# Optimization experiments

Hardware: AMD Instinct MI355X
Metric: run time of the kernel (lower is better)

The kernel has to match this reference:

```python
import jax, jax.numpy as jnp
import numpy as np

NUM_HEADS = 16
SOFTPLUS_EPS = 1e-4


def rotate_half(x):
    x1, x2 = jnp.split(x, 2, axis=-1)
    return jnp.concatenate((-x2, x1), axis=-1)


def setup_inputs() -> dict:
    key = jax.random.key(0)
    B, S, H = 1, 2048, 2048
    D = H // NUM_HEADS  # 128
    ks = jax.random.split(key, 5)
    hidden_states = jax.random.normal(ks[0], (B, S, H), dtype=jnp.float32)
    # standard RoPE tables: [S, D]
    inv_freq = 1.0 / (10000.0 ** (np.arange(0, D, 2, dtype=np.float32) / D))
    freqs = np.outer(np.arange(S, dtype=np.float32), inv_freq)  # [S, D/2]
    emb = np.concatenate([freqs, freqs], axis=-1)  # [S, D]
    cos = jnp.asarray(np.cos(emb), dtype=jnp.float32)
    sin = jnp.asarray(np.sin(emb), dtype=jnp.float32)
    std = 0.02
    w_q = jax.random.normal(ks[1], (2 * H, H), dtype=jnp.float32) * std
    w_k = jax.random.normal(ks[2], (2 * H, H), dtype=jnp.float32) * std
    w_v = jax.random.normal(ks[3], (H, H), dtype=jnp.float32) * std
    w_o = jax.random.normal(ks[4], (H, H), dtype=jnp.float32) * std
    return {"hidden_states": hidden_states, "cos": cos, "sin": sin,
            "w_q": w_q, "w_k": w_k, "w_v": w_v, "w_o": w_o}


def reference(hidden_states, cos, sin, w_q, w_k, w_v, w_o):
    B, S, H = hidden_states.shape
    NH = NUM_HEADS
    D = H // NH
    # projections (torch Linear: y = x @ W.T)
    q = (hidden_states @ w_q.T).reshape(B, S, NH, 2 * D).swapaxes(1, 2)  # [B,NH,S,2D]
    k = (hidden_states @ w_k.T).reshape(B, S, NH, 2 * D).swapaxes(1, 2)
    v = (hidden_states @ w_v.T).reshape(B, S, NH, D).swapaxes(1, 2)      # [B,NH,S,D]
    q_mu, q_sigma_raw = jnp.split(q, 2, axis=-1)
    k_mu, k_sigma_raw = jnp.split(k, 2, axis=-1)
    q_sigma = jax.nn.softplus(q_sigma_raw) + SOFTPLUS_EPS
    k_sigma = jax.nn.softplus(k_sigma_raw) + SOFTPLUS_EPS
    q_w = q_mu / jnp.sqrt(q_sigma)
    k_w = k_mu / jnp.sqrt(k_sigma)
    # RoPE on variance-weighted means; cos/sin [S,D] broadcast over [B,NH,S,D]
    q_w = q_w * cos + rotate_half(q_w) * sin
    k_w = k_w * cos + rotate_half(k_w) * sin
    q_sq = jnp.sum(q_w * q_w, axis=-1, keepdims=True)          # [B,NH,S,1]
    k_sq = jnp.sum(k_w * k_w, axis=-1, keepdims=True)          # [B,NH,S,1]
    dot = jnp.einsum('bhqd,bhkd->bhqk', q_w, k_w)              # [B,NH,S,S]
    weighted_dist = q_sq + jnp.swapaxes(k_sq, -2, -1) - 2.0 * dot
    log_det_q = jnp.sum(jnp.log(q_sigma), axis=-1, keepdims=True)
    log_det_k = jnp.sum(jnp.log(k_sigma), axis=-1, keepdims=True)
    log_det = log_det_q + jnp.swapaxes(log_det_k, -2, -1)
    attn_scores = -0.5 * (weighted_dist + log_det)
    attn_probs = jax.nn.softmax(attn_scores, axis=-1)
    attn_out = jnp.einsum('bhqk,bhkd->bhqd', attn_probs, v)    # [B,NH,S,D]
    attn_out = attn_out.swapaxes(1, 2).reshape(B, S, H)
    return attn_out @ w_o.T
```

## Files before the change

kernel.cpp:

```cpp
#include <hip/hip_runtime.h>
#include <stdint.h>

#define S_LEN 2048
#define HID   2048
#define NHEAD 16
#define HD    128
#define NQK   8192
#define K_HID 2048

typedef _Float16 f16x8 __attribute__((ext_vector_type(8)));
typedef float    f32x4 __attribute__((ext_vector_type(4)));

__device__ __forceinline__ unsigned short f2h(float f) {
    _Float16 h = (_Float16)f;
    union { _Float16 h; unsigned short u; } c; c.h = h;
    return c.u;
}
__device__ __forceinline__ float h2f(unsigned short b) {
    union { unsigned short u; _Float16 h; } c; c.u = b;
    return (float)c.h;
}
__device__ __forceinline__ float softplus_f(float x) {
    return (x > 20.f) ? x : log1pf(expf(x));
}
__device__ __forceinline__ void gload_lds16(const unsigned short* g, unsigned short* l) {
    __builtin_amdgcn_global_load_lds(
        (const __attribute__((address_space(1))) unsigned int*)g,
        (__attribute__((address_space(3))) unsigned int*)l, 16, 0, 0);
}
__device__ __forceinline__ void bar() {
    asm volatile("" ::: "memory");
    __builtin_amdgcn_s_barrier();
    asm volatile("" ::: "memory");
}
#define VMCNT(n) asm volatile("s_waitcnt vmcnt(" #n ")" ::: "memory")

__global__ __launch_bounds__(256) void cast5(const float* __restrict__ hs,
                                             const float* __restrict__ wq,
                                             const float* __restrict__ wk,
                                             const float* __restrict__ wv,
                                             const float* __restrict__ wo,
                                             unsigned short* __restrict__ hs16,
                                             unsigned short* __restrict__ wqk16,
                                             unsigned short* __restrict__ wv16,
                                             unsigned short* __restrict__ wo16) {
    int b = blockIdx.x;
    const float* src;
    unsigned short* dst;
    int i;
    if (b < 4096)       { src = hs; dst = hs16;                          i = b; }
    else if (b < 12288) { src = wq; dst = wqk16;                         i = b - 4096; }
    else if (b < 20480) { src = wk; dst = wqk16 + (size_t)4096 * K_HID;  i = b - 12288; }
    else if (b < 24576) { src = wv; dst = wv16;                          i = b - 20480; }
    else                { src = wo; dst = wo16;                          i = b - 24576; }
    int idx = i * 256 + threadIdx.x;
    float4 v = ((const float4*)src)[idx];
    ushort4 o;
    o.x = f2h(v.x); o.y = f2h(v.y); o.z = f2h(v.z); o.w = f2h(v.w);
    ((ushort4*)dst)[idx] = o;
}

template <bool OUT_F16>
__device__ __forceinline__ void gemm_body(const unsigned short* __restrict__ A,
                                          const unsigned short* __restrict__ B,
                                          void* __restrict__ Cv,
                                          int m0, int n0, int N,
                                          unsigned short* As, unsigned short* Bs) {
    const int t    = threadIdx.x;
    const int wave = t >> 6;
    const int lane = t & 63;
    const int wm   = wave >> 1, wn = wave & 1;
    const int lrow = lane & 15, quad = lane >> 4;
    const int srow = lane >> 2;
    const int scol = (lane & 3) * 8;

    f32x4 acc[4][4];
    for (int i = 0; i < 4; ++i)
        for (int j = 0; j < 4; ++j)
            acc[i][j] = (f32x4){0.f, 0.f, 0.f, 0.f};

    for (int k0 = 0; k0 < K_HID; k0 += 32) {
        for (int c = 0; c < 2; ++c) {
            int ch = wave * 2 + c;
            int row = ch * 16 + srow;
            gload_lds16(A + (size_t)(m0 + row) * K_HID + k0 + scol, &As[ch * 512]);
            gload_lds16(B + (size_t)(n0 + row) * K_HID + k0 + scol, &Bs[ch * 512]);
        }
        __syncthreads();

        f16x8 af[4], bfr[4];
        for (int tm = 0; tm < 4; ++tm)
            af[tm]  = *(const f16x8*)(&As[(wm * 64 + tm * 16 + lrow) * 32 + quad * 8]);
        for (int tn = 0; tn < 4; ++tn)
            bfr[tn] = *(const f16x8*)(&Bs[(wn * 64 + tn * 16 + lrow) * 32 + quad * 8]);
        for (int tm = 0; tm < 4; ++tm)
            for (int tn = 0; tn < 4; ++tn)
                acc[tm][tn] = __builtin_amdgcn_mfma_f32_16x16x32_f16(af[tm], bfr[tn], acc[tm][tn], 0, 0, 0);
        __syncthreads();
    }

    for (int tm = 0; tm < 4; ++tm)
        for (int tn = 0; tn < 4; ++tn) {
            int col = n0 + wn * 64 + tn * 16 + lrow;
            for (int r = 0; r < 4; ++r) {
                int row = m0 + wm * 64 + tm * 16 + quad * 4 + r;
                if (OUT_F16)
                    ((unsigned short*)Cv)[(size_t)row * N + col] = f2h(acc[tm][tn][r]);
                else
                    ((float*)Cv)[(size_t)row * N + col] = acc[tm][tn][r];
            }
        }
}

__global__ __launch_bounds__(256) void gemm_qkv(const unsigned short* __restrict__ hs16,
                                                const unsigned short* __restrict__ wqk16,
                                                const unsigned short* __restrict__ wv16,
                                                unsigned short* __restrict__ qk16,
                                                unsigned short* __restrict__ Vt) {
    __shared__ __align__(16) unsigned short As[128 * 32];
    __shared__ __align__(16) unsigned short Bs[128 * 32];
    int b = blockIdx.x;
    if (b < 1024) {
        gemm_body<true>(hs16, wqk16, qk16, (b >> 6) * 128, (b & 63) * 128, NQK, As, Bs);
    } else {
        b -= 1024;
        gemm_body<true>(wv16, hs16, Vt, (b >> 4) * 128, (b & 15) * 128, S_LEN, As, Bs);
    }
}

template <bool OUT_F16>
__global__ __launch_bounds__(256) void gemm_nt_f16(const unsigned short* __restrict__ A,
                                                   const unsigned short* __restrict__ B,
                                                   void* __restrict__ Cv,
                                                   int M, int N, int Kd) {
    __shared__ __align__(16) unsigned short As[128 * 32];
    __shared__ __align__(16) unsigned short Bs[128 * 32];
    gemm_body<OUT_F16>(A, B, Cv, blockIdx.y * 128, blockIdx.x * 128, N, As, Bs);
}

__global__ __launch_bounds__(512, 2) void gemm256_qk(const unsigned short* __restrict__ A,
                                                     const unsigned short* __restrict__ B,
                                                     unsigned short* __restrict__ C) {
    extern __shared__ __align__(16) unsigned short lds[];
    const int t    = threadIdx.x;
    const int wave = t >> 6;
    const int lane = t & 63;
    const int wm   = wave >> 2, wn = wave & 3;
    const int lrow = lane & 15, quad = lane >> 4;

    const int x  = blockIdx.x & 7;
    const int sl = blockIdx.x >> 3;
    const int tm = ((x >> 2) << 2) + (sl >> 3);
    const int tn = ((x & 3) << 3) + (sl & 7);
    const int m0 = tm << 8, n0 = tn << 8;

    const int srow = lane >> 2;
    const int scol = ((lane & 3) * 8) ^ ((lane >> 5) << 4);
    const unsigned short* Ag = A + (size_t)(m0 + wave * 16 + srow) * K_HID + scol;
    const unsigned short* Bg = B + (size_t)(n0 + wave * 16 + srow) * K_HID + scol;

    const int swz = (lrow * 32 + quad * 8) ^ ((lrow >> 3) << 4);

    f32x4 acc[8][4];
    #pragma unroll
    for (int i = 0; i < 8; ++i)
        #pragma unroll
        for (int j = 0; j < 4; ++j) acc[i][j] = (f32x4){0.f, 0.f, 0.f, 0.f};

    {
        unsigned short* la = lds + wave * 1024;
        gload_lds16(Ag,               la);
        gload_lds16(Ag + 32,          la + 512);
        gload_lds16(Ag + 262144,      la + 8192);
        gload_lds16(Ag + 262144 + 32, la + 8704);
        unsigned short* lb = la + 16384;
        gload_lds16(Bg,               lb);
        gload_lds16(Bg + 32,          lb + 512);
        gload_lds16(Bg + 262144,      lb + 8192);
        gload_lds16(Bg + 262144 + 32, lb + 8704);
    }
    VMCNT(0);
    bar();

    f16x8 ah[4][2], b01[2][2];

    const int NT = K_HID / 64;
    #pragma unroll 1
    for (int t2 = 0; t2 < NT; ++t2) {
        const int buf = t2 & 1;
        const unsigned short* Lb = lds + buf * 32768;
        unsigned short*       Ln = lds + (buf ^ 1) * 32768 + wave * 1024;
        const int k1  = (t2 + 1) * 64;
        const bool pre = (t2 < NT - 1);

        f16x8 al[4][2], b23[2][2];

        if (pre) {
            gload_lds16(Ag + k1,               Ln);
            gload_lds16(Ag + k1 + 32,          Ln + 512);
            gload_lds16(Ag + 262144 + k1,      Ln + 8192);
            gload_lds16(Ag + 262144 + k1 + 32, Ln + 8704);
        }
        #pragma unroll
        for (int i = 0; i < 4; ++i) {
            al[i][0] = *(const f16x8*)(Lb + (wm * 8 + i) * 1024 + swz);
            al[i][1] = *(const f16x8*)(Lb + (wm * 8 + i) * 1024 + 512 + swz);
        }
        if (t2) {
            __builtin_amdgcn_s_setprio(1);
            #pragma unroll
            for (int i = 0; i < 4; ++i)
                #pragma unroll
                for (int j = 0; j < 2; ++j) {
                    acc[4 + i][j] = __builtin_amdgcn_mfma_f32_16x16x32_f16(ah[i][0], b01[j][0], acc[4 + i][j], 0, 0, 0);
                    acc[4 + i][j] = __builtin_amdgcn_mfma_f32_16x16x32_f16(ah[i][1], b01[j][1], acc[4 + i][j], 0, 0, 0);
                }
            __builtin_amdgcn_s_setprio(0);
        }
        #pragma unroll
        for (int j = 0; j < 2; ++j) {
            b01[j][0] = *(const f16x8*)(Lb + 16384 + (wn * 4 + j) * 1024 + swz);
            b01[j][1] = *(const f16x8*)(Lb + 16384 + (wn * 4 + j) * 1024 + 512 + swz);
        }
        bar();

        if (pre) {
            gload_lds16(Bg + k1,               Ln + 16384);
            gload_lds16(Bg + k1 + 32,          Ln + 16896);
            gload_lds16(Bg + 262144 + k1,      Ln + 24576);
            gload_lds16(Bg + 262144 + k1 + 32, Ln + 25088);
        }
        #pragma unroll
        for (int j = 0; j < 2; ++j) {
            b23[j][0] = *(const f16x8*)(Lb + 16384 + (wn * 4 + 2 + j) * 1024 + swz);
            b23[j][1] = *(const f16x8*)(Lb + 16384 + (wn * 4 + 2 + j) * 1024 + 512 + swz);
        }
        __builtin_amdgcn_s_setprio(1);
        #pragma unroll
        for (int i = 0; i < 4; ++i)
            #pragma unroll
            for (int j = 0; j < 2; ++j) {
                acc[i][j] = __builtin_amdgcn_mfma_f32_16x16x32_f16(al[i][0], b01[j][0], acc[i][j], 0, 0, 0);
                acc[i][j] = __builtin_amdgcn_mfma_f32_16x16x32_f16(al[i][1], b01[j][1], acc[i][j], 0, 0, 0);
            }
        __builtin_amdgcn_s_setprio(0);
        bar();

        #pragma unroll
        for (int i = 0; i < 4; ++i) {
            ah[i][0] = *(const f16x8*)(Lb + (wm * 8 + 4 + i) * 1024 + swz);
            ah[i][1] = *(const f16x8*)(Lb + (wm * 8 + 4 + i) * 1024 + 512 + swz);
        }
        __builtin_amdgcn_s_setprio(1);
        #pragma unroll
        for (int i = 0; i < 4; ++i)
            #pragma unroll
            for (int j = 0; j < 2; ++j) {
                acc[i][2 + j] = __builtin_amdgcn_mfma_f32_16x16x32_f16(al[i][0], b23[j][0], acc[i][2 + j], 0, 0, 0);
                acc[i][2 + j] = __builtin_amdgcn_mfma_f32_16x16x32_f16(al[i][1], b23[j][1], acc[i][2 + j], 0, 0, 0);
            }
        __builtin_amdgcn_s_setprio(0);
        bar();

        __builtin_amdgcn_s_setprio(1);
        #pragma unroll
        for (int i = 0; i < 4; ++i)
            #pragma unroll
            for (int j = 0; j < 2; ++j) {
                acc[4 + i][2 + j] = __builtin_amdgcn_mfma_f32_16x16x32_f16(ah[i][0], b23[j][0], acc[4 + i][2 + j], 0, 0, 0);
                acc[4 + i][2 + j] = __builtin_amdgcn_mfma_f32_16x16x32_f16(ah[i][1], b23[j][1], acc[4 + i][2 + j], 0, 0, 0);
            }
        __builtin_amdgcn_s_setprio(0);
        VMCNT(0);
        bar();
    }

    __builtin_amdgcn_s_setprio(1);
    #pragma unroll
    for (int i = 0; i < 4; ++i)
        #pragma unroll
        for (int j = 0; j < 2; ++j) {
            acc[4 + i][j] = __builtin_amdgcn_mfma_f32_16x16x32_f16(ah[i][0], b01[j][0], acc[4 + i][j], 0, 0, 0);
            acc[4 + i][j] = __builtin_amdgcn_mfma_f32_16x16x32_f16(ah[i][1], b01[j][1], acc[4 + i][j], 0, 0, 0);
        }
    __builtin_amdgcn_s_setprio(0);

    #pragma unroll
    for (int m = 0; m < 8; ++m)
        #pragma unroll
        for (int n = 0; n < 4; ++n) {
            const int col = n0 + wn * 64 + n * 16 + lrow;
            #pragma unroll
            for (int r = 0; r < 4; ++r) {
                const int row = m0 + wm * 128 + m * 16 + quad * 4 + r;
                C[(size_t)row * NQK + col] = f2h(acc[m][n][r]);
            }
        }
}

__global__ __launch_bounds__(256) void prep_qk(const unsigned short* __restrict__ qk,
                                               const float* __restrict__ cosb,
                                               const float* __restrict__ sinb,
                                               unsigned short* __restrict__ Q16,
                                               unsigned short* __restrict__ K16,
                                               float* __restrict__ kbias) {
    int gid  = blockIdx.x * 4 + (threadIdx.x >> 6);
    int lane = threadIdx.x & 63;
    int h = gid >> 11;
    int s = gid & 2047;
    int d1 = lane, d2 = lane + 64;
    const unsigned short* row = qk + (size_t)s * NQK;
    float c1 = cosb[s * HD + d1], c2 = cosb[s * HD + d2];
    float s1 = sinb[s * HD + d1], s2 = sinb[s * HD + d2];
    size_t ob = ((size_t)h * S_LEN + s) * HD;

    {
        int base = h * 256;
        float mu1 = h2f(row[base + d1]),       mu2 = h2f(row[base + d2]);
        float sg1 = softplus_f(h2f(row[base + 128 + d1])) + 1e-4f;
        float sg2 = softplus_f(h2f(row[base + 128 + d2])) + 1e-4f;
        float w1 = mu1 * rsqrtf(sg1), w2 = mu2 * rsqrtf(sg2);
        float o1 = w1 * c1 - w2 * s1;
        float o2 = w2 * c2 + w1 * s2;
        Q16[ob + d1] = f2h(o1);
        Q16[ob + d2] = f2h(o2);
    }
    {
        int base = 4096 + h * 256;
        float mu1 = h2f(row[base + d1]),       mu2 = h2f(row[base + d2]);
        float sg1 = softplus_f(h2f(row[base + 128 + d1])) + 1e-4f;
        float sg2 = softplus_f(h2f(row[base + 128 + d2])) + 1e-4f;
        float w1 = mu1 * rsqrtf(sg1), w2 = mu2 * rsqrtf(sg2);
        float o1 = w1 * c1 - w2 * s1;
        float o2 = w2 * c2 + w1 * s2;
        unsigned short k1 = f2h(o1), k2 = f2h(o2);
        K16[ob + d1] = k1; K16[ob + d2] = k2;
        float r1 = h2f(k1), r2 = h2f(k2);
        float part = r1 * r1 + r2 * r2 + logf(sg1) + logf(sg2);
        for (int off = 32; off > 0; off >>= 1) part += __shfl_down(part, off);
        if (lane == 0) kbias[(size_t)h * S_LEN + s] = -0.5f * part;
    }
}

__global__ __launch_bounds__(256, 2) void flash_mfma(const unsigned short* __restrict__ Q16,
                                                     const unsigned short* __restrict__ K16,
                                                     const unsigned short* __restrict__ Vt,
                                                     const float* __restrict__ kbias,
                                                     unsigned short* __restrict__ OP,
                                                     float* __restrict__ ML) {
    constexpr int LV = 72;
    __shared__ __align__(16) unsigned short Khs[4 * 64 * 32];
    __shared__ __align__(16) unsigned short Vts[2 * 128 * 32];
    __shared__ __align__(16) unsigned short Ps[128 * LV];
    __shared__ float kb[64];

    const int t    = threadIdx.x;
    const int h    = blockIdx.y;
    const int q0   = blockIdx.x * 128;
    const int kz   = blockIdx.z;
    const int wave = t >> 6;
    const int lane = t & 63;
    const int lrow = lane & 15, quad = lane >> 4;
    const int srow = lane >> 2;
    const int scol = (lane & 3) * 8;

    f16x8 qf[2][4];
    for (int m = 0; m < 2; ++m) {
        size_t rb = ((size_t)h * S_LEN + q0 + wave * 32 + m * 16 + lrow) * HD;
        for (int kk = 0; kk < 4; ++kk)
            qf[m][kk] = *(const f16x8*)(Q16 + rb + kk * 32 + quad * 8);
    }

    float mrow[2][4], lsum[2][4];
    f32x4 Ofr[2][8];
    for (int m = 0; m < 2; ++m)
        for (int r = 0; r < 4; ++r) { mrow[m][r] = -INFINITY; lsum[m][r] = 0.f; }
    for (int m = 0; m < 2; ++m)
        for (int d = 0; d < 8; ++d) Ofr[m][d] = (f32x4){0.f, 0.f, 0.f, 0.f};

    const int kbeg = kz * 1024;
    for (int k0 = kbeg; k0 < kbeg + 1024; k0 += 64) {
        {
            const unsigned short* kgb = K16 + ((size_t)h * S_LEN + k0) * HD;
            const unsigned short* vgb = Vt + ((size_t)h * HD) * S_LEN + k0;
            for (int c = 0; c < 4; ++c) {
                int ch = wave * 4 + c;
                int kk = ch >> 2;
                int r  = (ch & 3) * 16 + srow;
                gload_lds16(kgb + (size_t)r * HD + kk * 32 + scol, &Khs[ch * 512]);
                int kc = ch >> 3;
                int r2 = (ch & 7) * 16 + srow;
                gload_lds16(vgb + (size_t)r2 * S_LEN + kc * 32 + scol, &Vts[ch * 512]);
            }
            if (t < 64) kb[t] = kbias[(size_t)h * S_LEN + k0 + t];
        }
        __syncthreads();

        f32x4 sc[2][4];
        for (int m = 0; m < 2; ++m)
            for (int nt = 0; nt < 4; ++nt) sc[m][nt] = (f32x4){0.f, 0.f, 0.f, 0.f};
        for (int kk = 0; kk < 4; ++kk)
            for (int nt = 0; nt < 4; ++nt) {
                f16x8 khf = *(const f16x8*)(&Khs[kk * 2048 + (nt * 16 + lrow) * 32 + quad * 8]);
                sc[0][nt] = __builtin_amdgcn_mfma_f32_16x16x32_f16(qf[0][kk], khf, sc[0][nt], 0, 0, 0);
                sc[1][nt] = __builtin_amdgcn_mfma_f32_16x16x32_f16(qf[1][kk], khf, sc[1][nt], 0, 0, 0);
            }
        float kbn[4] = {kb[lrow], kb[16 + lrow], kb[32 + lrow], kb[48 + lrow]};

        for (int m = 0; m < 2; ++m)
            for (int r = 0; r < 4; ++r) {
                float s0 = sc[m][0][r] + kbn[0];
                float s1 = sc[m][1][r] + kbn[1];
                float s2 = sc[m][2][r] + kbn[2];
                float s3 = sc[m][3][r] + kbn[3];
                float mx = fmaxf(fmaxf(s0, s1), fmaxf(s2, s3));
                mx = fmaxf(mx, __shfl_xor(mx, 1));
                mx = fmaxf(mx, __shfl_xor(mx, 2));
                mx = fmaxf(mx, __shfl_xor(mx, 4));
                mx = fmaxf(mx, __shfl_xor(mx, 8));
                float mnew  = fmaxf(mrow[m][r], mx);
                float alpha = __expf(mrow[m][r] - mnew);
                mrow[m][r] = mnew;
                float p0 = __expf(s0 - mnew);
                float p1 = __expf(s1 - mnew);
                float p2 = __expf(s2 - mnew);
                float p3 = __expf(s3 - mnew);
                lsum[m][r] = lsum[m][r] * alpha + ((p0 + p1) + (p2 + p3));
                for (int d = 0; d < 8; ++d) Ofr[m][d][r] *= alpha;
                int prow = (wave * 32 + m * 16 + quad * 4 + r) * LV;
                Ps[prow + lrow]      = f2h(p0);
                Ps[prow + 16 + lrow] = f2h(p1);
                Ps[prow + 32 + lrow] = f2h(p2);
                Ps[prow + 48 + lrow] = f2h(p3);
            }

        for (int c = 0; c < 2; ++c) {
            f16x8 pa0 = *(const f16x8*)(&Ps[(wave * 32 + lrow) * LV + c * 32 + quad * 8]);
            f16x8 pa1 = *(const f16x8*)(&Ps[(wave * 32 + 16 + lrow) * LV + c * 32 + quad * 8]);
            for (int dt = 0; dt < 8; ++dt) {
                f16x8 vb = *(const f16x8*)(&Vts[c * 4096 + (dt * 16 + lrow) * 32 + quad * 8]);
                Ofr[0][dt] = __builtin_amdgcn_mfma_f32_16x16x32_f16(pa0, vb, Ofr[0][dt], 0, 0, 0);
                Ofr[1][dt] = __builtin_amdgcn_mfma_f32_16x16x32_f16(pa1, vb, Ofr[1][dt], 0, 0, 0);
            }
        }
        __syncthreads();
    }

    size_t obase = (size_t)(kz * NHEAD + h) * S_LEN;
    for (int m = 0; m < 2; ++m)
        for (int r = 0; r < 4; ++r) {
            float rs = lsum[m][r];
            rs += __shfl_xor(rs, 1);
            rs += __shfl_xor(rs, 2);
            rs += __shfl_xor(rs, 4);
            rs += __shfl_xor(rs, 8);
            int qrow = q0 + wave * 32 + m * 16 + quad * 4 + r;
            unsigned short* op = OP + (obase + qrow) * HD;
            for (int dt = 0; dt < 8; ++dt)
                op[dt * 16 + lrow] = f2h(Ofr[m][dt][r]);
            if (lrow == 0) {
                ML[(obase + qrow) * 2]     = mrow[m][r];
                ML[(obase + qrow) * 2 + 1] = rs;
            }
        }
}

__global__ __launch_bounds__(256) void flash_merge(const unsigned short* __restrict__ OP,
                                                   const float* __restrict__ ML,
                                                   unsigned short* __restrict__ Obf) {
    int row = blockIdx.x * 2 + (threadIdx.x >> 7);
    int d   = threadIdx.x & 127;
    int h = row >> 11, q = row & 2047;
    size_t i0 = (size_t)h * S_LEN + q;
    size_t i1 = (size_t)(NHEAD + h) * S_LEN + q;
    float m0 = ML[i0 * 2], l0 = ML[i0 * 2 + 1];
    float m1 = ML[i1 * 2], l1 = ML[i1 * 2 + 1];
    float mf = fmaxf(m0, m1);
    float w0 = __expf(m0 - mf), w1 = __expf(m1 - mf);
    float inv = 1.f / (l0 * w0 + l1 * w1);
    float o = (h2f(OP[i0 * HD + d]) * w0 + h2f(OP[i1 * HD + d]) * w1) * inv;
    Obf[(size_t)q * HID + h * HD + d] = f2h(o);
}

extern "C" void kernel_launch(void* const* d_in, const int* in_sizes, int n_in,
                              void* d_out, int out_size, void* d_ws, size_t ws_size,
                              hipStream_t stream) {
    const float* hs   = (const float*)d_in[0];
    const float* cosb = (const float*)d_in[1];
    const float* sinb = (const float*)d_in[2];
    const float* wq   = (const float*)d_in[3];
    const float* wk   = (const float*)d_in[4];
    const float* wv   = (const float*)d_in[5];
    const float* wo   = (const float*)d_in[6];
    float* out = (float*)d_out;
    char*  ws  = (char*)d_ws;

    unsigned short* w_qk16 = (unsigned short*)(ws);
    unsigned short* Q16    = (unsigned short*)(ws);
    unsigned short* K16    = (unsigned short*)(ws + 8388608);
    float*          kbias  = (float*)(ws + 16777216);
    unsigned short* qk16   = (unsigned short*)(ws + 33554432);
    unsigned short* OP     = (unsigned short*)(ws + 33554432);
    float*          ML     = (float*)(ws + 50331648);
    unsigned short* hs16   = (unsigned short*)(ws + 67108864);
    unsigned short* Obf    = (unsigned short*)(ws + 67108864);
    unsigned short* w_v16  = (unsigned short*)(ws + 75497472);
    unsigned short* w_o16  = (unsigned short*)(ws + 83886080);
    unsigned short* Vt     = (unsigned short*)(ws + 92274688);

    static int use256 = -1;
    if (use256 < 0) {
        hipError_t e = hipFuncSetAttribute((const void*)gemm256_qk,
                                           hipFuncAttributeMaxDynamicSharedMemorySize,
                                           131072);
        use256 = (e == hipSuccess) ? 1 : 0;
    }

    cast5<<<28672, 256, 0, stream>>>(hs, wq, wk, wv, wo, hs16, w_qk16, w_v16, w_o16);

    if (use256) {
        gemm256_qk<<<256, 512, 131072, stream>>>(hs16, w_qk16, qk16);
        gemm_nt_f16<true><<<dim3(16, 16), 256, 0, stream>>>(w_v16, hs16, Vt, HID, S_LEN, K_HID);
    } else {
        gemm_qkv<<<1280, 256, 0, stream>>>(hs16, w_qk16, w_v16, qk16, Vt);
    }

    prep_qk<<<(NHEAD * S_LEN) / 4, 256, 0, stream>>>(qk16, cosb, sinb,
                                                     Q16, K16, kbias);
    flash_mfma<<<dim3(S_LEN / 128, NHEAD, 2), 256, 0, stream>>>(Q16, K16, Vt,
                                                                kbias, OP, ML);
    flash_merge<<<(NHEAD * S_LEN) / 2, 256, 0, stream>>>(OP, ML, Obf);
    gemm_nt_f16<false><<<dim3(16, 16), 256, 0, stream>>>(Obf, w_o16, out, S_LEN, HID, K_HID);
}
```

Before: 389.3 us.

## Transpose score MFMA, fold log2e into Q/bias, and swizzle flash block order

Swaps MFMA operands so each lane holds one query row's scores, which reduces the softmax max/sum reductions to two cross-quad shuffles and lets P be written to LDS as packed half pairs. Log2(e) is folded into Q and the key bias so the softmax can use the native exp2 instruction, and the merge kernel switches to exp2 to match. The flash grid is flattened to 1D with a remapped block index that groups heads and key-splits, meant to improve cache reuse of K/V. In exchange, alpha must be broadcast with shuffles to rescale the output accumulators, and Q is rounded to fp16 after scaling by log2(e).

```diff
diff --git a/kernel.cpp b/kernel.cpp
--- a/kernel.cpp
+++ b/kernel.cpp
@@ -23,6 +23,13 @@
 __device__ __forceinline__ float softplus_f(float x) {
     return (x > 20.f) ? x : log1pf(expf(x));
 }
+__device__ __forceinline__ unsigned pk2h(float a, float b) {
+    auto w = __builtin_amdgcn_cvt_pkrtz(a, b);
+    union { decltype(w) h; unsigned u; } c; c.h = w;
+    return c.u;
+}
+#define EXP2F(x) __builtin_amdgcn_exp2f(x)
+#define LOG2E 1.44269504088896f
 __device__ __forceinline__ void gload_lds16(const unsigned short* g, unsigned short* l) {
     __builtin_amdgcn_global_load_lds(
         (const __attribute__((address_space(1))) unsigned int*)g,
@@ -322,8 +329,8 @@
         float w1 = mu1 * rsqrtf(sg1), w2 = mu2 * rsqrtf(sg2);
         float o1 = w1 * c1 - w2 * s1;
         float o2 = w2 * c2 + w1 * s2;
-        Q16[ob + d1] = f2h(o1);
-        Q16[ob + d2] = f2h(o2);
+        Q16[ob + d1] = f2h(o1 * LOG2E);
+        Q16[ob + d2] = f2h(o2 * LOG2E);
     }
     {
         int base = 4096 + h * 256;
@@ -338,7 +345,7 @@
         float r1 = h2f(k1), r2 = h2f(k2);
         float part = r1 * r1 + r2 * r2 + logf(sg1) + logf(sg2);
         for (int off = 32; off > 0; off >>= 1) part += __shfl_down(part, off);
-        if (lane == 0) kbias[(size_t)h * S_LEN + s] = -0.5f * part;
+        if (lane == 0) kbias[(size_t)h * S_LEN + s] = -0.5f * LOG2E * part;
     }
 }
 
@@ -355,9 +362,11 @@
     __shared__ float kb[64];
 
     const int t    = threadIdx.x;
-    const int h    = blockIdx.y;
-    const int q0   = blockIdx.x * 128;
-    const int kz   = blockIdx.z;
+    const int bb   = blockIdx.x;
+    const int cc   = (bb & 7) | (((bb >> 7) & 3) << 3);
+    const int h    = cc & 15;
+    const int kz   = cc >> 4;
+    const int q0   = ((bb >> 3) & 15) * 128;
     const int wave = t >> 6;
     const int lane = t & 63;
     const int lrow = lane & 15, quad = lane >> 4;
@@ -371,10 +380,9 @@
             qf[m][kk] = *(const f16x8*)(Q16 + rb + kk * 32 + quad * 8);
     }
 
-    float mrow[2][4], lsum[2][4];
+    float mrow[2], lsum[2];
     f32x4 Ofr[2][8];
-    for (int m = 0; m < 2; ++m)
-        for (int r = 0; r < 4; ++r) { mrow[m][r] = -INFINITY; lsum[m][r] = 0.f; }
+    for (int m = 0; m < 2; ++m) { mrow[m] = -INFINITY; lsum[m] = 0.f; }
     for (int m = 0; m < 2; ++m)
         for (int d = 0; d < 8; ++d) Ofr[m][d] = (f32x4){0.f, 0.f, 0.f, 0.f};
 
@@ -402,37 +410,62 @@
         for (int kk = 0; kk < 4; ++kk)
             for (int nt = 0; nt < 4; ++nt) {
                 f16x8 khf = *(const f16x8*)(&Khs[kk * 2048 + (nt * 16 + lrow) * 32 + quad * 8]);
-                sc[0][nt] = __builtin_amdgcn_mfma_f32_16x16x32_f16(qf[0][kk], khf, sc[0][nt], 0, 0, 0);
-                sc[1][nt] = __builtin_amdgcn_mfma_f32_16x16x32_f16(qf[1][kk], khf, sc[1][nt], 0, 0, 0);
-            }
-        float kbn[4] = {kb[lrow], kb[16 + lrow], kb[32 + lrow], kb[48 + lrow]};
-
-        for (int m = 0; m < 2; ++m)
-            for (int r = 0; r < 4; ++r) {
-                float s0 = sc[m][0][r] + kbn[0];
-                float s1 = sc[m][1][r] + kbn[1];
-                float s2 = sc[m][2][r] + kbn[2];
-                float s3 = sc[m][3][r] + kbn[3];
-                float mx = fmaxf(fmaxf(s0, s1), fmaxf(s2, s3));
-                mx = fmaxf(mx, __shfl_xor(mx, 1));
-                mx = fmaxf(mx, __shfl_xor(mx, 2));
-                mx = fmaxf(mx, __shfl_xor(mx, 4));
-                mx = fmaxf(mx, __shfl_xor(mx, 8));
-                float mnew  = fmaxf(mrow[m][r], mx);
-                float alpha = __expf(mrow[m][r] - mnew);
-                mrow[m][r] = mnew;
-                float p0 = __expf(s0 - mnew);
-                float p1 = __expf(s1 - mnew);
-                float p2 = __expf(s2 - mnew);
-                float p3 = __expf(s3 - mnew);
-                lsum[m][r] = lsum[m][r] * alpha + ((p0 + p1) + (p2 + p3));
-                for (int d = 0; d < 8; ++d) Ofr[m][d][r] *= alpha;
-                int prow = (wave * 32 + m * 16 + quad * 4 + r) * LV;
-                Ps[prow + lrow]      = f2h(p0);
-                Ps[prow + 16 + lrow] = f2h(p1);
-                Ps[prow + 32 + lrow] = f2h(p2);
-                Ps[prow + 48 + lrow] = f2h(p3);
-            }
+                sc[0][nt] = __builtin_amdgcn_mfma_f32_16x16x32_f16(khf, qf[0][kk], sc[0][nt], 0, 0, 0);
+                sc[1][nt] = __builtin_amdgcn_mfma_f32_16x16x32_f16(khf, qf[1][kk], sc[1][nt], 0, 0, 0);
+            }
+
+        f32x4 kbv[4];
+        #pragma unroll
+        for (int nt = 0; nt < 4; ++nt)
+            kbv[nt] = *(const f32x4*)(&kb[nt * 16 + quad * 4]);
+
+        #pragma unroll
+        for (int m = 0; m < 2; ++m) {
+            float s[4][4];
+            float mx = -INFINITY;
+            #pragma unroll
+            for (int nt = 0; nt < 4; ++nt)
+                #pragma unroll
+                for (int r = 0; r < 4; ++r) {
+                    s[nt][r] = sc[m][nt][r] + kbv[nt][r];
+                    mx = fmaxf(mx, s[nt][r]);
+                }
+            mx = fmaxf(mx, __shfl_xor(mx, 16));
+            mx = fmaxf(mx, __shfl_xor(mx, 32));
+            float mnew  = fmaxf(mrow[m], mx);
+            float alpha = EXP2F(mrow[m] - mnew);
+            mrow[m] = mnew;
+            float psum = 0.f;
+            unsigned pw[8];
+            #pragma unroll
+            for (int nt = 0; nt < 4; ++nt) {
+                float p0 = EXP2F(s[nt][0] - mnew);
+                float p1 = EXP2F(s[nt][1] - mnew);
+                float p2 = EXP2F(s[nt][2] - mnew);
+                float p3 = EXP2F(s[nt][3] - mnew);
+                psum += (p0 + p1) + (p2 + p3);
+                pw[nt * 2]     = pk2h(p0, p1);
+                pw[nt * 2 + 1] = pk2h(p2, p3);
+            }
+            lsum[m] = lsum[m] * alpha + psum;
+            float av0 = __shfl(alpha, quad * 4 + 0);
+            float av1 = __shfl(alpha, quad * 4 + 1);
+            float av2 = __shfl(alpha, quad * 4 + 2);
+            float av3 = __shfl(alpha, quad * 4 + 3);
+            #pragma unroll
+            for (int dt = 0; dt < 8; ++dt) {
+                Ofr[m][dt][0] *= av0;
+                Ofr[m][dt][1] *= av1;
+                Ofr[m][dt][2] *= av2;
+                Ofr[m][dt][3] *= av3;
+            }
+            int prow = (wave * 32 + m * 16 + lrow) * LV;
+            #pragma unroll
+            for (int nt = 0; nt < 4; ++nt) {
+                uint2 wv; wv.x = pw[nt * 2]; wv.y = pw[nt * 2 + 1];
+                *(uint2*)(&Ps[prow + nt * 16 + quad * 4]) = wv;
+            }
+        }
 
         for (int c = 0; c < 2; ++c) {
             f16x8 pa0 = *(const f16x8*)(&Ps[(wave * 32 + lrow) * LV + c * 32 + quad * 8]);
@@ -447,22 +480,22 @@
     }
 
     size_t obase = (size_t)(kz * NHEAD + h) * S_LEN;
-    for (int m = 0; m < 2; ++m)
+    for (int m = 0; m < 2; ++m) {
+        float rs = lsum[m];
+        rs += __shfl_xor(rs, 16);
+        rs += __shfl_xor(rs, 32);
+        if (quad == 0) {
+            int qrow = q0 + wave * 32 + m * 16 + lrow;
+            ML[(obase + qrow) * 2]     = mrow[m];
+            ML[(obase + qrow) * 2 + 1] = rs;
+        }
         for (int r = 0; r < 4; ++r) {
-            float rs = lsum[m][r];
-            rs += __shfl_xor(rs, 1);
-            rs += __shfl_xor(rs, 2);
-            rs += __shfl_xor(rs, 4);
-            rs += __shfl_xor(rs, 8);
             int qrow = q0 + wave * 32 + m * 16 + quad * 4 + r;
             unsigned short* op = OP + (obase + qrow) * HD;
             for (int dt = 0; dt < 8; ++dt)
                 op[dt * 16 + lrow] = f2h(Ofr[m][dt][r]);
-            if (lrow == 0) {
-                ML[(obase + qrow) * 2]     = mrow[m][r];
-                ML[(obase + qrow) * 2 + 1] = rs;
-            }
-        }
+        }
+    }
 }
 
 __global__ __launch_bounds__(256) void flash_merge(const unsigned short* __restrict__ OP,
@@ -476,7 +509,7 @@
     float m0 = ML[i0 * 2], l0 = ML[i0 * 2 + 1];
     float m1 = ML[i1 * 2], l1 = ML[i1 * 2 + 1];
     float mf = fmaxf(m0, m1);
-    float w0 = __expf(m0 - mf), w1 = __expf(m1 - mf);
+    float w0 = EXP2F(m0 - mf), w1 = EXP2F(m1 - mf);
     float inv = 1.f / (l0 * w0 + l1 * w1);
     float o = (h2f(OP[i0 * HD + d]) * w0 + h2f(OP[i1 * HD + d]) * w1) * inv;
     Obf[(size_t)q * HID + h * HD + d] = f2h(o);
@@ -527,8 +560,7 @@
 
     prep_qk<<<(NHEAD * S_LEN) / 4, 256, 0, stream>>>(qk16, cosb, sinb,
                                                      Q16, K16, kbias);
-    flash_mfma<<<dim3(S_LEN / 128, NHEAD, 2), 256, 0, stream>>>(Q16, K16, Vt,
-                                                                kbias, OP, ML);
+    flash_mfma<<<512, 256, 0, stream>>>(Q16, K16, Vt, kbias, OP, ML);
     flash_merge<<<(NHEAD * S_LEN) / 2, 256, 0, stream>>>(OP, ML, Obf);
     gemm_nt_f16<false><<<dim3(16, 16), 256, 0, stream>>>(Obf, w_o16, out, S_LEN, HID, K_HID);
 }
```

New measurement: 379.6 us (median of 2 runs). -2.5%, faster.
